# Kernel optimization log

Hardware: AMD Instinct MI355X
Metric: run time of the kernel (lower is better)

Reference implementation:

```python
import jax, jax.numpy as jnp
import numpy as np

EMBED_DIM = 512
N_HEAD = 8
Q_DIM = 64
V_DIM = 64
WINDOW_SIZE = 3


def setup_inputs() -> dict:
    key = jax.random.key(0)
    ks = jax.random.split(key, 9)
    B, N = 2, 2048
    x = jax.random.normal(ks[0], (B, N, EMBED_DIM), dtype=jnp.float32)
    s = 0.02
    # torch nn.Linear weights are [out_features, in_features]; y = x @ W.T + b
    Wq = jax.random.normal(ks[1], (N_HEAD * Q_DIM, EMBED_DIM), dtype=jnp.float32) * s
    bq = jax.random.normal(ks[2], (N_HEAD * Q_DIM,), dtype=jnp.float32) * s
    Wk = jax.random.normal(ks[3], (N_HEAD * Q_DIM, EMBED_DIM), dtype=jnp.float32) * s
    bk = jax.random.normal(ks[4], (N_HEAD * Q_DIM,), dtype=jnp.float32) * s
    Wv = jax.random.normal(ks[5], (N_HEAD * V_DIM, EMBED_DIM), dtype=jnp.float32) * s
    bv = jax.random.normal(ks[6], (N_HEAD * V_DIM,), dtype=jnp.float32) * s
    Wo = jax.random.normal(ks[7], (EMBED_DIM, N_HEAD * V_DIM), dtype=jnp.float32) * s
    bo = jax.random.normal(ks[8], (EMBED_DIM,), dtype=jnp.float32) * s
    return {"x": x, "Wq": Wq, "bq": bq, "Wk": Wk, "bk": bk,
            "Wv": Wv, "bv": bv, "Wo": Wo, "bo": bo}


def _diag_indices(n_seq, di):
    # rows i and cols j = i + di of the di-th diagonal
    if di >= 0:
        ii = np.arange(0, n_seq - di)
    else:
        ii = np.arange(-di, n_seq)
    return ii, ii + di


def reference(x, Wq, bq, Wk, bk, Wv, bv, Wo, bo):
    B, N, E = x.shape
    H, Dq, Dv = N_HEAD, Q_DIM, V_DIM
    Q = (x @ Wq.T + bq).reshape(B, N, H, Dq).transpose(0, 2, 1, 3)  # [B,H,N,Dq]
    K = (x @ Wk.T + bk).reshape(B, N, H, Dq).transpose(0, 2, 1, 3)
    V = (x @ Wv.T + bv).reshape(B, N, H, Dv).transpose(0, 2, 1, 3)  # [B,H,N,Dv]
    half = WINDOW_SIZE // 2
    # Faithful to source: scores scattered into COLUMN index i (the loop
    # counter), not the key position; all other columns remain 0 and still
    # participate in the full softmax over n_seq.
    columns = jnp.zeros((B, H, N, N), dtype=x.dtype)
    for i, di in enumerate(range(-half, half + 1)):
        ii, jj = _diag_indices(N, di)
        c = jnp.einsum('bhid,bhid->bhi', Q[:, :, ii, :], K[:, :, jj, :])
        columns = columns.at[:, :, ii, i].set(c)
    attn = jax.nn.softmax(columns, axis=-1)          # [B,H,N,N]
    out = attn @ V                                    # [B,H,N,Dv]
    out = out.transpose(0, 2, 1, 3).reshape(B, N, H * Dv)
    return out @ Wo.T + bo
```

## Files before the change

kernel.cpp:

```cpp
#include <hip/hip_runtime.h>
#include <hip/hip_bf16.h>

#define EMBED 512
#define NSEQ 2048
#define NROWS 4096

typedef unsigned short u16;
typedef __bf16 bf16x8 __attribute__((ext_vector_type(8)));
typedef float f32x4 __attribute__((ext_vector_type(4)));
typedef unsigned short ushort8 __attribute__((ext_vector_type(8)));

__device__ __forceinline__ u16 f2bf(float f) {
    unsigned u = __float_as_uint(f);
    unsigned r = (u + 0x7FFFu + ((u >> 16) & 1u)) >> 16;
    return (u16)r;
}
__device__ __forceinline__ float bf2f(u16 v) {
    return __uint_as_float((unsigned)v << 16);
}

#define XELEMS    (NROWS * EMBED)
#define WQKELEMS  (1024 * EMBED)

__global__ __launch_bounds__(256) void prep_kernel(
    const float* __restrict__ x,
    const float* __restrict__ Wq, const float* __restrict__ Wk,
    u16* __restrict__ xb, u16* __restrict__ Wcat,
    float* __restrict__ xcs_part)
{
    __shared__ float cs[4][512];
    const int bid = blockIdx.x, t = threadIdx.x;
    if (bid < 256) {
        const float* src = x + (size_t)bid * 16 * EMBED;
        u16* dst = xb + (size_t)bid * 16 * EMBED;
        const int rl = t >> 6;
        const int co = (t & 63) * 8;
        float s0=0.f,s1=0.f,s2=0.f,s3=0.f,s4=0.f,s5=0.f,s6=0.f,s7=0.f;
#pragma unroll
        for (int i = 0; i < 4; ++i) {
            const size_t off = (size_t)(i * 4 + rl) * EMBED + co;
            float4 a = *(const float4*)(src + off);
            float4 b = *(const float4*)(src + off + 4);
            union { u16 u[8]; uint4 v; } p;
            p.u[0]=f2bf(a.x); p.u[1]=f2bf(a.y); p.u[2]=f2bf(a.z); p.u[3]=f2bf(a.w);
            p.u[4]=f2bf(b.x); p.u[5]=f2bf(b.y); p.u[6]=f2bf(b.z); p.u[7]=f2bf(b.w);
            *(uint4*)(dst + off) = p.v;
            s0+=a.x; s1+=a.y; s2+=a.z; s3+=a.w;
            s4+=b.x; s5+=b.y; s6+=b.z; s7+=b.w;
        }
        f32x4 v0 = {s0,s1,s2,s3}, v1 = {s4,s5,s6,s7};
        *(f32x4*)&cs[rl][co]     = v0;
        *(f32x4*)&cs[rl][co + 4] = v1;
        __syncthreads();
        const int b = bid >> 7, blk = bid & 127;
#pragma unroll
        for (int d = t; d < 512; d += 256) {
            xcs_part[((size_t)b * 128 + blk) * 512 + d] =
                cs[0][d] + cs[1][d] + cs[2][d] + cs[3][d];
        }
    } else {
        const long long e0 = (long long)(bid - 256) * 2048 + (long long)t * 8;
        const int row = (int)(e0 >> 9), col = (int)(e0 & 511);
        const float* src = (row < 512) ? (Wq + (size_t)row * EMBED + col)
                                       : (Wk + (size_t)(row - 512) * EMBED + col);
        float4 a = *(const float4*)(src);
        float4 b = *(const float4*)(src + 4);
        union { u16 u[8]; uint4 v; } p;
        p.u[0]=f2bf(a.x); p.u[1]=f2bf(a.y); p.u[2]=f2bf(a.z); p.u[3]=f2bf(a.w);
        p.u[4]=f2bf(b.x); p.u[5]=f2bf(b.y); p.u[6]=f2bf(b.z); p.u[7]=f2bf(b.w);
        *(uint4*)(Wcat + e0) = p.v;
    }
}

__global__ __launch_bounds__(256) void gemm_qk_mfma(
    const u16* __restrict__ A, const u16* __restrict__ W,
    const float* __restrict__ bq, const float* __restrict__ bk,
    const float* __restrict__ xcs_part, const float* __restrict__ bv,
    const float* __restrict__ Wv, const float* __restrict__ Wo,
    u16* __restrict__ QKb, float* __restrict__ WT)
{
    __shared__ __align__(16) u16 As[128 * 64];
    __shared__ __align__(16) u16 Bs[64 * 64];
    const int t = threadIdx.x;

    if (blockIdx.x < 32) {
        float* xcs  = (float*)As;
        float* Vraw = (float*)Bs;
        float* Vloc = Vraw + 256;
        const int sid = blockIdx.x;
        const int b = sid >> 4, h = (sid >> 1) & 7, jhalf = sid & 1;

        {
            const float* p = xcs_part + (size_t)b * 128 * 512 + 2 * t;
            float a0 = 0.f, a1 = 0.f, c0 = 0.f, c1 = 0.f;
#pragma unroll 4
            for (int blk = 0; blk < 128; blk += 2) {
                float2 u = *(const float2*)(p + (size_t)blk * 512);
                float2 v = *(const float2*)(p + (size_t)(blk + 1) * 512);
                a0 += u.x; a1 += u.y; c0 += v.x; c1 += v.y;
            }
            xcs[2 * t] = a0 + c0; xcs[2 * t + 1] = a1 + c1;
        }
        __syncthreads();

        const int tt = t >> 6, cl = t & 63;
        const int col = h * 64 + cl;
        const float* wv = Wv + (size_t)col * EMBED;
        float r = 0.f;
        if (tt < 3) {
            const u16* xr = A + ((size_t)b * NSEQ + tt) * EMBED;
#pragma unroll 8
            for (int d = 0; d < EMBED; d += 8) {
                ushort8 xv = *(const ushort8*)(xr + d);
                f32x4 w0 = *(const f32x4*)(wv + d);
                f32x4 w1 = *(const f32x4*)(wv + d + 4);
                r = fmaf(bf2f(xv[0]), w0[0], r);
                r = fmaf(bf2f(xv[1]), w0[1], r);
                r = fmaf(bf2f(xv[2]), w0[2], r);
                r = fmaf(bf2f(xv[3]), w0[3], r);
                r = fmaf(bf2f(xv[4]), w1[0], r);
                r = fmaf(bf2f(xv[5]), w1[1], r);
                r = fmaf(bf2f(xv[6]), w1[2], r);
                r = fmaf(bf2f(xv[7]), w1[3], r);
            }
        } else {
#pragma unroll 8
            for (int d = 0; d < EMBED; d += 4) {
                f32x4 w = *(const f32x4*)(wv + d);
                r = fmaf(xcs[d],     w[0], r);
                r = fmaf(xcs[d + 1], w[1], r);
                r = fmaf(xcs[d + 2], w[2], r);
                r = fmaf(xcs[d + 3], w[3], r);
            }
        }
        Vraw[tt * 64 + cl] = r;
        __syncthreads();
        const float bvc = bv[col];
        if (tt < 3) Vloc[tt * 64 + cl] = r + bvc;
        else        Vloc[192 + cl] = r - (Vraw[cl] + Vraw[64 + cl] + Vraw[128 + cl])
                                       + 2045.f * bvc;
        __syncthreads();

        const int j = jhalf * 256 + t;
        const float* wo = Wo + (size_t)j * EMBED + h * 64;
        float a0 = 0.f, a1 = 0.f, a2 = 0.f, a3 = 0.f;
#pragma unroll
        for (int c = 0; c < 64; c += 4) {
            f32x4 w = *(const f32x4*)(wo + c);
#pragma unroll
            for (int z = 0; z < 4; ++z) {
                a0 = fmaf(Vloc[c + z],       w[z], a0);
                a1 = fmaf(Vloc[64 + c + z],  w[z], a1);
                a2 = fmaf(Vloc[128 + c + z], w[z], a2);
                a3 = fmaf(Vloc[192 + c + z], w[z], a3);
            }
        }
        float* wt = WT + ((size_t)b * 512 + j) * 32 + h * 4;
        wt[0] = a0; wt[1] = a1; wt[2] = a2; wt[3] = a3;
        return;
    }

    const int bb = blockIdx.x - 32;
    const int m0 = (bb & 31) * 128;
    const int n0 = (bb >> 5) * 64;
    const int sel = n0 >> 9;
    const float* bias = ((sel == 0) ? bq : bk) + (n0 & 511);

    const int wave = t >> 6, lane = t & 63;
    const int wm   = wave >> 1, wn = wave & 1;
    const int qd   = lane >> 4, lr = lane & 15;

    const int sr8 = lane >> 3;
    const int sg  = (lane & 7) ^ sr8;
    const int soff = sg * 8;

    f32x4 acc[4][2] = {};

    const u16* Ag = A + (size_t)m0 * EMBED;
    const u16* Wg = W + (size_t)n0 * EMBED;

    u16* Adst = As + (size_t)(wave * 8) * 64;
    u16* Bdst = Bs + (size_t)(wave * 8) * 64;
    const u16* Asrc = Ag + (size_t)(wave * 8 + sr8) * EMBED + soff;
    const u16* Bsrc = Wg + (size_t)(wave * 8 + sr8) * EMBED + soff;

    for (int kc = 0; kc < EMBED; kc += 64) {
#pragma unroll
        for (int j = 0; j < 4; ++j)
            __builtin_amdgcn_global_load_lds(
                (const __attribute__((address_space(1))) void*)(Asrc + kc + (size_t)j * 32 * EMBED),
                (__attribute__((address_space(3))) void*)(Adst + j * 32 * 64), 16, 0, 0);
#pragma unroll
        for (int j = 0; j < 2; ++j)
            __builtin_amdgcn_global_load_lds(
                (const __attribute__((address_space(1))) void*)(Bsrc + kc + (size_t)j * 32 * EMBED),
                (__attribute__((address_space(3))) void*)(Bdst + j * 32 * 64), 16, 0, 0);
        __syncthreads();

#pragma unroll
        for (int kk = 0; kk < 2; ++kk) {
            const int gr = ((kk * 4 + qd) ^ (lr & 7)) * 8;
            bf16x8 af[4], bfr[2];
#pragma unroll
            for (int i = 0; i < 4; ++i)
                af[i]  = *(const bf16x8*)&As[(wm * 64 + i * 16 + lr) * 64 + gr];
#pragma unroll
            for (int i = 0; i < 2; ++i)
                bfr[i] = *(const bf16x8*)&Bs[(wn * 32 + i * 16 + lr) * 64 + gr];
#pragma unroll
            for (int mi = 0; mi < 4; ++mi)
#pragma unroll
                for (int ni = 0; ni < 2; ++ni)
                    acc[mi][ni] = __builtin_amdgcn_mfma_f32_16x16x32_bf16(
                        af[mi], bfr[ni], acc[mi][ni], 0, 0, 0);
        }
        __syncthreads();
    }

#pragma unroll
    for (int ni = 0; ni < 2; ++ni) {
        const int cl = wn * 32 + ni * 16 + lr;
        const float bb2 = bias[cl];
#pragma unroll
        for (int mi = 0; mi < 4; ++mi)
#pragma unroll
            for (int e = 0; e < 4; ++e) {
                const int row = m0 + wm * 64 + mi * 16 + qd * 4 + e;
                QKb[(size_t)row * 1024 + n0 + cl] = f2bf(acc[mi][ni][e] + bb2);
            }
    }
}

__global__ __launch_bounds__(256) void attn_out_kernel(
    const u16* __restrict__ QKb, const float* __restrict__ WT,
    const float* __restrict__ bo, float* __restrict__ out)
{
    __shared__ float E[16][32];
    const int r0   = blockIdx.x * 16;
    const int b    = r0 >> 11;
    const int wave = threadIdx.x >> 6, lane = threadIdx.x & 63;
    const int d0   = lane * 8;

#pragma unroll
    for (int i = 0; i < 4; ++i) {
        const int rl = wave * 4 + i;
        const int r  = r0 + rl;
        const int sr = r & (NSEQ - 1);
        const u16* Qr = QKb + (size_t)r * 1024 + d0;
        const u16* Kr = QKb + (size_t)r * 1024 + 512 + d0;

        ushort8 qv = *(const ushort8*)Qr;
        ushort8 kv = *(const ushort8*)Kr;
        float q[8], k[8];
#pragma unroll
        for (int z = 0; z < 8; ++z) { q[z] = bf2f(qv[z]); k[z] = bf2f(kv[z]); }

        float s1 = 0.f;
#pragma unroll
        for (int z = 0; z < 8; ++z) s1 = fmaf(q[z], k[z], s1);

        float s0 = 0.f, s2 = 0.f;
        if (sr > 0) {
            ushort8 pv = *(const ushort8*)(Kr - 1024);
#pragma unroll
            for (int z = 0; z < 8; ++z) s0 = fmaf(q[z], bf2f(pv[z]), s0);
        }
        if (sr < NSEQ - 1) {
            ushort8 nv = *(const ushort8*)(Kr + 1024);
#pragma unroll
            for (int z = 0; z < 8; ++z) s2 = fmaf(q[z], bf2f(nv[z]), s2);
        }
#pragma unroll
        for (int off = 1; off <= 4; off <<= 1) {
            s0 += __shfl_xor(s0, off);
            s1 += __shfl_xor(s1, off);
            s2 += __shfl_xor(s2, off);
        }
        const float m  = fmaxf(fmaxf(s0, s1), fmaxf(s2, 0.f));
        const float e0 = __expf(s0 - m);
        const float e1 = __expf(s1 - m);
        const float e2 = __expf(s2 - m);
        const float eb = __expf(-m);
        const float rd = 1.f / (e0 + e1 + e2 + (float)(NSEQ - 3) * eb);
        const int h = lane >> 3, jj = lane & 7;
        const float coef = (jj == 0) ? e0 : (jj == 1) ? e1 : (jj == 2) ? e2 : eb;
        if (jj < 4) E[rl][h * 4 + jj] = coef * rd;
    }
    __syncthreads();

    const int j0 = threadIdx.x * 2;
    const float* WTb = WT + (size_t)b * 512 * 32;
    float w0[32], w1[32];
#pragma unroll
    for (int s = 0; s < 32; ++s) {
        w0[s] = WTb[(size_t)j0 * 32 + s];
        w1[s] = WTb[(size_t)(j0 + 1) * 32 + s];
    }
    const float b0 = bo[j0], b1 = bo[j0 + 1];
#pragma unroll
    for (int rl = 0; rl < 16; ++rl) {
        float a0 = b0, a1 = b1;
#pragma unroll
        for (int s = 0; s < 32; ++s) {
            const float e = E[rl][s];
            a0 = fmaf(e, w0[s], a0);
            a1 = fmaf(e, w1[s], a1);
        }
        *(float2*)(out + (size_t)(r0 + rl) * EMBED + j0) = make_float2(a0, a1);
    }
}

extern "C" void kernel_launch(void* const* d_in, const int* in_sizes, int n_in,
                              void* d_out, int out_size, void* d_ws, size_t ws_size,
                              hipStream_t stream)
{
    const float* x  = (const float*)d_in[0];
    const float* Wq = (const float*)d_in[1];
    const float* bq = (const float*)d_in[2];
    const float* Wk = (const float*)d_in[3];
    const float* bk = (const float*)d_in[4];
    const float* Wv = (const float*)d_in[5];
    const float* bv = (const float*)d_in[6];
    const float* Wo = (const float*)d_in[7];
    const float* bo = (const float*)d_in[8];
    float* out = (float*)d_out;

    u16*   QKb      = (u16*)d_ws;
    u16*   xb       = QKb + (size_t)NROWS * 1024;
    u16*   Wcat     = xb + XELEMS;
    float* xcs_part = (float*)(Wcat + WQKELEMS);
    float* WT       = xcs_part + 2 * 128 * 512;

    prep_kernel<<<512, 256, 0, stream>>>(x, Wq, Wk, xb, Wcat, xcs_part);
    gemm_qk_mfma<<<544, 256, 0, stream>>>(xb, Wcat, bq, bk, xcs_part, bv, Wv, Wo,
                                          QKb, WT);
    attn_out_kernel<<<256, 256, 0, stream>>>(QKb, WT, bo, out);
}
```

Before: 117.5 us.

## Split V-path work into separate kernel and restructure prep into flat conversion plus column sums

The prep kernel now converts x and Wq/Wk to bf16 in a flat elementwise grid, and computes x column sums in 64 separate blocks that each read 64-row chunks. The column sums are therefore reduced from 32 partials per batch instead of 128. The V/Wo precomputation moves out of the GEMM launch into its own 32-block kernel, so GEMM blocks no longer share a grid with those long-running blocks. The cost is an extra kernel launch, and x is now read twice, once for conversion and once for the sums.

After: 121.6 us. +3.6%, slower.

```diff
diff --git a/kernel.cpp b/kernel.cpp
--- a/kernel.cpp
+++ b/kernel.cpp
@@ -28,141 +28,135 @@
     u16* __restrict__ xb, u16* __restrict__ Wcat,
     float* __restrict__ xcs_part)
 {
-    __shared__ float cs[4][512];
     const int bid = blockIdx.x, t = threadIdx.x;
-    if (bid < 256) {
-        const float* src = x + (size_t)bid * 16 * EMBED;
-        u16* dst = xb + (size_t)bid * 16 * EMBED;
-        const int rl = t >> 6;
-        const int co = (t & 63) * 8;
-        float s0=0.f,s1=0.f,s2=0.f,s3=0.f,s4=0.f,s5=0.f,s6=0.f,s7=0.f;
-#pragma unroll
-        for (int i = 0; i < 4; ++i) {
-            const size_t off = (size_t)(i * 4 + rl) * EMBED + co;
-            float4 a = *(const float4*)(src + off);
-            float4 b = *(const float4*)(src + off + 4);
-            union { u16 u[8]; uint4 v; } p;
-            p.u[0]=f2bf(a.x); p.u[1]=f2bf(a.y); p.u[2]=f2bf(a.z); p.u[3]=f2bf(a.w);
-            p.u[4]=f2bf(b.x); p.u[5]=f2bf(b.y); p.u[6]=f2bf(b.z); p.u[7]=f2bf(b.w);
-            *(uint4*)(dst + off) = p.v;
-            s0+=a.x; s1+=a.y; s2+=a.z; s3+=a.w;
-            s4+=b.x; s5+=b.y; s6+=b.z; s7+=b.w;
-        }
-        f32x4 v0 = {s0,s1,s2,s3}, v1 = {s4,s5,s6,s7};
-        *(f32x4*)&cs[rl][co]     = v0;
-        *(f32x4*)&cs[rl][co + 4] = v1;
-        __syncthreads();
-        const int b = bid >> 7, blk = bid & 127;
-#pragma unroll
-        for (int d = t; d < 512; d += 256) {
-            xcs_part[((size_t)b * 128 + blk) * 512 + d] =
-                cs[0][d] + cs[1][d] + cs[2][d] + cs[3][d];
-        }
-    } else {
-        const long long e0 = (long long)(bid - 256) * 2048 + (long long)t * 8;
-        const int row = (int)(e0 >> 9), col = (int)(e0 & 511);
-        const float* src = (row < 512) ? (Wq + (size_t)row * EMBED + col)
-                                       : (Wk + (size_t)(row - 512) * EMBED + col);
+    if (bid < 1280) {
+        const float* src;
+        u16* dst;
+        if (bid < 1024) {
+            const long long e0 = (long long)bid * 2048 + (long long)t * 8;
+            src = x + e0; dst = xb + e0;
+        } else {
+            const long long j = (long long)(bid - 1024) * 2048 + (long long)t * 8;
+            const int row = (int)(j >> 9), col = (int)(j & 511);
+            src = (row < 512) ? (Wq + (size_t)row * EMBED + col)
+                              : (Wk + (size_t)(row - 512) * EMBED + col);
+            dst = Wcat + j;
+        }
         float4 a = *(const float4*)(src);
         float4 b = *(const float4*)(src + 4);
         union { u16 u[8]; uint4 v; } p;
         p.u[0]=f2bf(a.x); p.u[1]=f2bf(a.y); p.u[2]=f2bf(a.z); p.u[3]=f2bf(a.w);
         p.u[4]=f2bf(b.x); p.u[5]=f2bf(b.y); p.u[6]=f2bf(b.z); p.u[7]=f2bf(b.w);
-        *(uint4*)(Wcat + e0) = p.v;
-    }
+        *(uint4*)(dst) = p.v;
+    } else {
+        const int cid   = bid - 1280;
+        const int b     = cid >> 5;
+        const int chunk = cid & 31;
+        const float* p = x + ((size_t)b * NSEQ + (size_t)chunk * 64) * EMBED + 2 * t;
+        float a0 = 0.f, a1 = 0.f, c0 = 0.f, c1 = 0.f;
+#pragma unroll 8
+        for (int rr = 0; rr < 64; rr += 2) {
+            float2 u = *(const float2*)(p + (size_t)rr * EMBED);
+            float2 v = *(const float2*)(p + (size_t)(rr + 1) * EMBED);
+            a0 += u.x; a1 += u.y; c0 += v.x; c1 += v.y;
+        }
+        float2 o = make_float2(a0 + c0, a1 + c1);
+        *(float2*)(xcs_part + ((size_t)(b * 32 + chunk) * 512) + 2 * t) = o;
+    }
+}
+
+__global__ __launch_bounds__(256) void vsmall_kernel(
+    const u16* __restrict__ xb, const float* __restrict__ xcs_part,
+    const float* __restrict__ bv, const float* __restrict__ Wv,
+    const float* __restrict__ Wo, float* __restrict__ WT)
+{
+    __shared__ float xcs[512];
+    __shared__ float Vraw[4][64];
+    __shared__ float Vloc[4][64];
+    const int t = threadIdx.x;
+    const int sid = blockIdx.x;
+    const int b = sid >> 4, h = (sid >> 1) & 7, jhalf = sid & 1;
+
+    {
+        const float* p = xcs_part + (size_t)b * 32 * 512 + 2 * t;
+        float a0 = 0.f, a1 = 0.f, c0 = 0.f, c1 = 0.f;
+#pragma unroll
+        for (int ch = 0; ch < 32; ch += 2) {
+            float2 u = *(const float2*)(p + (size_t)ch * 512);
+            float2 v = *(const float2*)(p + (size_t)(ch + 1) * 512);
+            a0 += u.x; a1 += u.y; c0 += v.x; c1 += v.y;
+        }
+        xcs[2 * t] = a0 + c0; xcs[2 * t + 1] = a1 + c1;
+    }
+    __syncthreads();
+
+    const int tt = t >> 6, cl = t & 63;
+    const int col = h * 64 + cl;
+    const float* wv = Wv + (size_t)col * EMBED;
+    float r = 0.f;
+    if (tt < 3) {
+        const u16* xr = xb + ((size_t)b * NSEQ + tt) * EMBED;
+#pragma unroll 8
+        for (int d = 0; d < EMBED; d += 8) {
+            ushort8 xv = *(const ushort8*)(xr + d);
+            f32x4 w0 = *(const f32x4*)(wv + d);
+            f32x4 w1 = *(const f32x4*)(wv + d + 4);
+            r = fmaf(bf2f(xv[0]), w0[0], r);
+            r = fmaf(bf2f(xv[1]), w0[1], r);
+            r = fmaf(bf2f(xv[2]), w0[2], r);
+            r = fmaf(bf2f(xv[3]), w0[3], r);
+            r = fmaf(bf2f(xv[4]), w1[0], r);
+            r = fmaf(bf2f(xv[5]), w1[1], r);
+            r = fmaf(bf2f(xv[6]), w1[2], r);
+            r = fmaf(bf2f(xv[7]), w1[3], r);
+        }
+    } else {
+#pragma unroll 8
+        for (int d = 0; d < EMBED; d += 4) {
+            f32x4 w = *(const f32x4*)(wv + d);
+            r = fmaf(xcs[d],     w[0], r);
+            r = fmaf(xcs[d + 1], w[1], r);
+            r = fmaf(xcs[d + 2], w[2], r);
+            r = fmaf(xcs[d + 3], w[3], r);
+        }
+    }
+    Vraw[tt][cl] = r;
+    __syncthreads();
+    const float bvc = bv[col];
+    if (tt < 3) Vloc[tt][cl] = r + bvc;
+    else        Vloc[3][cl] = r - (Vraw[0][cl] + Vraw[1][cl] + Vraw[2][cl])
+                                + 2045.f * bvc;
+    __syncthreads();
+
+    const int j = jhalf * 256 + t;
+    const float* wo = Wo + (size_t)j * EMBED + h * 64;
+    float a0 = 0.f, a1 = 0.f, a2 = 0.f, a3 = 0.f;
+#pragma unroll
+    for (int c = 0; c < 64; c += 4) {
+        f32x4 w = *(const f32x4*)(wo + c);
+#pragma unroll
+        for (int z = 0; z < 4; ++z) {
+            a0 = fmaf(Vloc[0][c + z], w[z], a0);
+            a1 = fmaf(Vloc[1][c + z], w[z], a1);
+            a2 = fmaf(Vloc[2][c + z], w[z], a2);
+            a3 = fmaf(Vloc[3][c + z], w[z], a3);
+        }
+    }
+    float* wt = WT + ((size_t)b * 512 + j) * 32 + h * 4;
+    wt[0] = a0; wt[1] = a1; wt[2] = a2; wt[3] = a3;
 }
 
 __global__ __launch_bounds__(256) void gemm_qk_mfma(
     const u16* __restrict__ A, const u16* __restrict__ W,
     const float* __restrict__ bq, const float* __restrict__ bk,
-    const float* __restrict__ xcs_part, const float* __restrict__ bv,
-    const float* __restrict__ Wv, const float* __restrict__ Wo,
-    u16* __restrict__ QKb, float* __restrict__ WT)
+    u16* __restrict__ QKb)
 {
     __shared__ __align__(16) u16 As[128 * 64];
     __shared__ __align__(16) u16 Bs[64 * 64];
     const int t = threadIdx.x;
 
-    if (blockIdx.x < 32) {
-        float* xcs  = (float*)As;
-        float* Vraw = (float*)Bs;
-        float* Vloc = Vraw + 256;
-        const int sid = blockIdx.x;
-        const int b = sid >> 4, h = (sid >> 1) & 7, jhalf = sid & 1;
-
-        {
-            const float* p = xcs_part + (size_t)b * 128 * 512 + 2 * t;
-            float a0 = 0.f, a1 = 0.f, c0 = 0.f, c1 = 0.f;
-#pragma unroll 4
-            for (int blk = 0; blk < 128; blk += 2) {
-                float2 u = *(const float2*)(p + (size_t)blk * 512);
-                float2 v = *(const float2*)(p + (size_t)(blk + 1) * 512);
-                a0 += u.x; a1 += u.y; c0 += v.x; c1 += v.y;
-            }
-            xcs[2 * t] = a0 + c0; xcs[2 * t + 1] = a1 + c1;
-        }
-        __syncthreads();
-
-        const int tt = t >> 6, cl = t & 63;
-        const int col = h * 64 + cl;
-        const float* wv = Wv + (size_t)col * EMBED;
-        float r = 0.f;
-        if (tt < 3) {
-            const u16* xr = A + ((size_t)b * NSEQ + tt) * EMBED;
-#pragma unroll 8
-            for (int d = 0; d < EMBED; d += 8) {
-                ushort8 xv = *(const ushort8*)(xr + d);
-                f32x4 w0 = *(const f32x4*)(wv + d);
-                f32x4 w1 = *(const f32x4*)(wv + d + 4);
-                r = fmaf(bf2f(xv[0]), w0[0], r);
-                r = fmaf(bf2f(xv[1]), w0[1], r);
-                r = fmaf(bf2f(xv[2]), w0[2], r);
-                r = fmaf(bf2f(xv[3]), w0[3], r);
-                r = fmaf(bf2f(xv[4]), w1[0], r);
-                r = fmaf(bf2f(xv[5]), w1[1], r);
-                r = fmaf(bf2f(xv[6]), w1[2], r);
-                r = fmaf(bf2f(xv[7]), w1[3], r);
-            }
-        } else {
-#pragma unroll 8
-            for (int d = 0; d < EMBED; d += 4) {
-                f32x4 w = *(const f32x4*)(wv + d);
-                r = fmaf(xcs[d],     w[0], r);
-                r = fmaf(xcs[d + 1], w[1], r);
-                r = fmaf(xcs[d + 2], w[2], r);
-                r = fmaf(xcs[d + 3], w[3], r);
-            }
-        }
-        Vraw[tt * 64 + cl] = r;
-        __syncthreads();
-        const float bvc = bv[col];
-        if (tt < 3) Vloc[tt * 64 + cl] = r + bvc;
-        else        Vloc[192 + cl] = r - (Vraw[cl] + Vraw[64 + cl] + Vraw[128 + cl])
-                                       + 2045.f * bvc;
-        __syncthreads();
-
-        const int j = jhalf * 256 + t;
-        const float* wo = Wo + (size_t)j * EMBED + h * 64;
-        float a0 = 0.f, a1 = 0.f, a2 = 0.f, a3 = 0.f;
-#pragma unroll
-        for (int c = 0; c < 64; c += 4) {
-            f32x4 w = *(const f32x4*)(wo + c);
-#pragma unroll
-            for (int z = 0; z < 4; ++z) {
-                a0 = fmaf(Vloc[c + z],       w[z], a0);
-                a1 = fmaf(Vloc[64 + c + z],  w[z], a1);
-                a2 = fmaf(Vloc[128 + c + z], w[z], a2);
-                a3 = fmaf(Vloc[192 + c + z], w[z], a3);
-            }
-        }
-        float* wt = WT + ((size_t)b * 512 + j) * 32 + h * 4;
-        wt[0] = a0; wt[1] = a1; wt[2] = a2; wt[3] = a3;
-        return;
-    }
-
-    const int bb = blockIdx.x - 32;
-    const int m0 = (bb & 31) * 128;
-    const int n0 = (bb >> 5) * 64;
+    const int m0 = (blockIdx.x & 31) * 128;
+    const int n0 = (blockIdx.x >> 5) * 64;
     const int sel = n0 >> 9;
     const float* bias = ((sel == 0) ? bq : bk) + (n0 & 511);
 
@@ -220,13 +214,13 @@
 #pragma unroll
     for (int ni = 0; ni < 2; ++ni) {
         const int cl = wn * 32 + ni * 16 + lr;
-        const float bb2 = bias[cl];
+        const float bb = bias[cl];
 #pragma unroll
         for (int mi = 0; mi < 4; ++mi)
 #pragma unroll
             for (int e = 0; e < 4; ++e) {
                 const int row = m0 + wm * 64 + mi * 16 + qd * 4 + e;
-                QKb[(size_t)row * 1024 + n0 + cl] = f2bf(acc[mi][ni][e] + bb2);
+                QKb[(size_t)row * 1024 + n0 + cl] = f2bf(acc[mi][ni][e] + bb);
             }
     }
 }
@@ -329,10 +323,10 @@
     u16*   xb       = QKb + (size_t)NROWS * 1024;
     u16*   Wcat     = xb + XELEMS;
     float* xcs_part = (float*)(Wcat + WQKELEMS);
-    float* WT       = xcs_part + 2 * 128 * 512;
-
-    prep_kernel<<<512, 256, 0, stream>>>(x, Wq, Wk, xb, Wcat, xcs_part);
-    gemm_qk_mfma<<<544, 256, 0, stream>>>(xb, Wcat, bq, bk, xcs_part, bv, Wv, Wo,
-                                          QKb, WT);
+    float* WT       = xcs_part + 2 * 32 * 512;
+
+    prep_kernel<<<1344, 256, 0, stream>>>(x, Wq, Wk, xb, Wcat, xcs_part);
+    vsmall_kernel<<<32, 256, 0, stream>>>(xb, xcs_part, bv, Wv, Wo, WT);
+    gemm_qk_mfma<<<512, 256, 0, stream>>>(xb, Wcat, bq, bk, QKb);
     attn_out_kernel<<<256, 256, 0, stream>>>(QKb, WT, bo, out);
 }
```
